# Optimization experiments

Hardware: AMD Instinct MI355X
Metric: run time of the kernel (lower is better)

## Reference

```python
import jax, jax.numpy as jnp
import numpy as np


def setup_inputs() -> dict:
    key = jax.random.key(0)
    k1, k2, k3 = jax.random.split(key, 3)
    T, H, F, E = 8192, 1024, 4096, 8
    x = jax.random.normal(k1, (T, H), dtype=jnp.float32)
    # expert weights, scaled like typical init (std ~ 1/sqrt(H))
    w1 = jax.random.normal(k2, (E, F, H), dtype=jnp.float32) * (1.0 / np.sqrt(H))
    w2 = jax.random.normal(k3, (E, F, H), dtype=jnp.float32) * (1.0 / np.sqrt(F))
    return {"x": x, "w1": w1, "w2": w2, "num_experts": E}


def reference(x, w1, w2, num_experts):
    # x: [T, H] tokens already permuted/grouped by expert (dMoE convention),
    # equal capacity per expert. w1, w2: [E, F, H].
    T, H = x.shape
    E = num_experts
    cap = T // E
    xe = x.reshape(E, cap, H)  # [E, cap, H]
    # sdd(x, w1.t(), topo): per-expert x_e @ w1_e^T -> [E, cap, F]
    h = jnp.einsum('ech,efh->ecf', xe, w1)
    # megablocks uses tanh-approximate gelu
    h = jax.nn.gelu(h, approximate=True)
    # dsd(gelu(h), w2): per-expert h_e @ w2_e -> [E, cap, H]
    out = jnp.einsum('ecf,efh->ech', h, w2)
    return out.reshape(T, H)
```

## Files before the change

kernel.cpp:

```cpp
#include <hip/hip_runtime.h>
#include <cstdint>
#include <cstddef>

typedef unsigned short u16;
typedef __attribute__((ext_vector_type(8))) short bf16x8;
typedef __attribute__((ext_vector_type(4))) float f32x4;
typedef __attribute__((ext_vector_type(8))) unsigned short u16x8;

#define T_TOK 8192
#define H_DIM 1024
#define F_DIM 4096
#define E_NUM 8
#define CAP (T_TOK / E_NUM)

__device__ __forceinline__ u16 f2bf(float f) {
  union { float f; uint32_t u; } v; v.f = f;
  uint32_t r = v.u + 0x7FFFu + ((v.u >> 16) & 1u);
  return (u16)(r >> 16);
}

__device__ __forceinline__ float gelu_tanh(float x) {
  float z2 = 1.5957691216057308f * (x + 0.044715f * x * x * x);
  float e = __expf(z2);
  return x * (1.0f - 1.0f / (e + 1.0f));
}

__device__ __forceinline__ void async_copy16(const void* gsrc, void* ldst) {
  __builtin_amdgcn_global_load_lds(
      (const __attribute__((address_space(1))) uint32_t*)gsrc,
      (__attribute__((address_space(3))) uint32_t*)ldst, 16, 0, 0);
}

__device__ __forceinline__ void wgbar() {
  asm volatile("" ::: "memory");
  __builtin_amdgcn_s_barrier();
  asm volatile("" ::: "memory");
}

template <int N> __device__ __forceinline__ void vm_wait() {
  if constexpr (N == 0) asm volatile("s_waitcnt vmcnt(0)" ::: "memory");
  else if constexpr (N == 3) asm volatile("s_waitcnt vmcnt(3)" ::: "memory");
  else if constexpr (N == 4) asm volatile("s_waitcnt vmcnt(4)" ::: "memory");
}

__global__ __launch_bounds__(256) void k_convert(const float* __restrict__ src,
                                                 u16* __restrict__ dst, long n) {
  long i = ((long)blockIdx.x * 256 + threadIdx.x) * 8;
  long stride = (long)gridDim.x * 256 * 8;
  for (; i < n; i += stride) {
    const float4 a = *(const float4*)(src + i);
    const float4 b = *(const float4*)(src + i + 4);
    u16x8 o;
    o[0] = f2bf(a.x); o[1] = f2bf(a.y); o[2] = f2bf(a.z); o[3] = f2bf(a.w);
    o[4] = f2bf(b.x); o[5] = f2bf(b.y); o[6] = f2bf(b.z); o[7] = f2bf(b.w);
    *(u16x8*)(dst + i) = o;
  }
}

__global__ __launch_bounds__(256) void k_transpose_w2(const float* __restrict__ w2,
                                                      u16* __restrict__ w2t) {
  __shared__ float tile[32][33];
  const int ntH = H_DIM / 32;
  const int ntF = F_DIM / 32;
  int bid = blockIdx.x;
  int e = bid / (ntF * ntH);
  int r = bid % (ntF * ntH);
  int f0 = (r / ntH) * 32;
  int h0 = (r % ntH) * 32;
  const float* src = w2 + (size_t)e * F_DIM * H_DIM;
  u16* dst = w2t + (size_t)e * H_DIM * F_DIM;
  int col = threadIdx.x & 31;
  int row8 = threadIdx.x >> 5;
#pragma unroll
  for (int i = 0; i < 4; i++) {
    int row = row8 + i * 8;
    tile[row][col] = src[(size_t)(f0 + row) * H_DIM + h0 + col];
  }
  __syncthreads();
#pragma unroll
  for (int i = 0; i < 4; i++) {
    int row = row8 + i * 8;
    dst[(size_t)(h0 + row) * F_DIM + f0 + col] = f2bf(tile[col][row]);
  }
}

template <int BN, int WM, int WN, int NTM, int NTN, int NT, bool GELU>
__global__ __launch_bounds__(512, 2) void k_gemm8(const u16* __restrict__ Ag,
                                                  const u16* __restrict__ Bg,
                                                  void* __restrict__ Cg) {
  constexpr int K = NT * 64;
  constexpr int FM = 256 / (WM * 16);
  constexpr int FN = BN / (WN * 16);
  constexpr int FMH = FM / 2;
  constexpr int PA = 256 * 32;
  constexpr int PB = BN * 32;
  constexpr int ABOFF = 4 * PA;
  constexpr int BSTG = (BN * 32 * 2) / (512 * 16);
  constexpr int VMC = 2 + BSTG;
  constexpr int NTOT = NTN * BN;

  __shared__ __align__(16) u16 lds[ABOFF + 4 * PB];

  const int tid = threadIdx.x;
  const int lane = tid & 63;
  const int wave = tid >> 6;
  const int wm = wave / WN;
  const int wn = wave % WN;

  constexpr int NWG = NTM * NTN;
  const int wg = ((int)blockIdx.x & 7) * (NWG / 8) + ((int)blockIdx.x >> 3);
  constexpr int NSN = NTN / 4;
  const int sup = wg >> 4, win = wg & 15;
  const int mt = (sup / NSN) * 4 + (win >> 2);
  const int nt_ = (sup % NSN) * 4 + (win & 3);

  const int e = mt >> 2;
  const u16* Ae = Ag + (size_t)mt * 256 * K;
  const u16* Be = Bg + (size_t)e * NTOT * K + (size_t)nt_ * BN * K;

  const int srow = lane >> 2;
  const int kswz = (((lane & 3) ^ ((lane >> 3) & 3)) << 3);

  auto stageA = [&](int t, int kh) {
    u16* dst0 = &lds[((t & 1) * 2 + kh) * PA];
    const u16* src = Ae + (size_t)(t * 64 + kh * 32 + kswz);
#pragma unroll
    for (int j = 0; j < 2; ++j) {
      const int cr = (2 * wave + j) * 16 + srow;
      async_copy16(src + (size_t)cr * K, dst0 + (2 * wave + j) * 512);
    }
  };
  auto stageB = [&](int t, int kh) {
    u16* dst0 = &lds[ABOFF + ((t & 1) * 2 + kh) * PB];
    const u16* src = Be + (size_t)(t * 64 + kh * 32 + kswz);
#pragma unroll
    for (int j = 0; j < BSTG; ++j) {
      const int cr = (BSTG * wave + j) * 16 + srow;
      async_copy16(src + (size_t)cr * K, dst0 + (BSTG * wave + j) * 512);
    }
  };

  const int frow = lane & 15;
  const int fslot = (((lane >> 4) ^ ((lane >> 1) & 3)) << 3);

  f32x4 acc[FM][FN] = {};

  stageA(0, 0); stageB(0, 0); stageA(0, 1); stageB(0, 1);
  stageA(1, 0); stageB(1, 0);
  vm_wait<VMC>();
  wgbar();

  for (int t = 0; t < NT; ++t) {
    const bool s01 = (t < NT - 1);
    const bool s23 = (t < NT - 2);
    bf16x8 af[FMH], bfr[FN];
#pragma unroll
    for (int q = 0; q < 4; ++q) {
      const int kh = q >> 1, mh = q & 1;
      const u16* pa = &lds[((t & 1) * 2 + kh) * PA];
      const u16* pb = &lds[ABOFF + ((t & 1) * 2 + kh) * PB];
      if (mh == 0) {
#pragma unroll
        for (int i = 0; i < FN; ++i) {
          const int r = wn * (BN / WN) + i * 16 + frow;
          bfr[i] = *(const bf16x8*)&pb[r * 32 + fslot];
        }
      }
#pragma unroll
      for (int i = 0; i < FMH; ++i) {
        const int r = wm * (256 / WM) + (mh * FMH + i) * 16 + frow;
        af[i] = *(const bf16x8*)&pa[r * 32 + fslot];
      }
      if (q == 0) { if (s01) stageA(t + 1, 1); }
      else if (q == 1) { if (s01) stageB(t + 1, 1); }
      else if (q == 2) { if (s23) stageA(t + 2, 0); }
      else { if (s23) stageB(t + 2, 0); }
      wgbar();
      asm volatile("s_waitcnt lgkmcnt(0)" ::: "memory");
      __builtin_amdgcn_sched_barrier(0);
      __builtin_amdgcn_s_setprio(1);
#pragma unroll
      for (int i = 0; i < FMH; ++i)
#pragma unroll
        for (int fn = 0; fn < FN; ++fn)
          acc[mh * FMH + i][fn] = __builtin_amdgcn_mfma_f32_16x16x32_bf16(
              af[i], bfr[fn], acc[mh * FMH + i][fn], 0, 0, 0);
      __builtin_amdgcn_s_setprio(0);
      if (q == 3) {
        if (s23) vm_wait<VMC>(); else vm_wait<0>();
      }
      wgbar();
    }
  }

  const int lr = (lane >> 4) * 4;
  const int lc = lane & 15;
  const size_t Crow0 = (size_t)mt * 256 + wm * (256 / WM);
  const int Ccol0 = nt_ * BN + wn * (BN / WN);
  if constexpr (GELU) {
    u16* Cp = (u16*)Cg;
#pragma unroll
    for (int fm = 0; fm < FM; ++fm)
#pragma unroll
      for (int fn = 0; fn < FN; ++fn) {
        const int col = Ccol0 + fn * 16 + lc;
#pragma unroll
        for (int r = 0; r < 4; ++r) {
          const size_t row = Crow0 + fm * 16 + lr + r;
          Cp[row * NTOT + col] = f2bf(gelu_tanh(acc[fm][fn][r]));
        }
      }
  } else {
    float* Cp = (float*)Cg;
#pragma unroll
    for (int fm = 0; fm < FM; ++fm)
#pragma unroll
      for (int fn = 0; fn < FN; ++fn) {
        const int col = Ccol0 + fn * 16 + lc;
#pragma unroll
        for (int r = 0; r < 4; ++r) {
          const size_t row = Crow0 + fm * 16 + lr + r;
          Cp[row * NTOT + col] = acc[fm][fn][r];
        }
      }
  }
}

extern "C" void kernel_launch(void* const* d_in, const int* in_sizes, int n_in,
                              void* d_out, int out_size, void* d_ws, size_t ws_size,
                              hipStream_t stream) {
  const float* x = (const float*)d_in[0];
  const float* w1 = (const float*)d_in[1];
  const float* w2 = (const float*)d_in[2];

  u16* ws_x = (u16*)d_ws;
  u16* ws_w1 = ws_x + (size_t)T_TOK * H_DIM;
  u16* ws_w2t = ws_w1 + (size_t)E_NUM * F_DIM * H_DIM;
  u16* ws_h = ws_w2t + (size_t)E_NUM * H_DIM * F_DIM;
  const size_t need =
      ((size_t)T_TOK * H_DIM + 2 * (size_t)E_NUM * F_DIM * H_DIM + (size_t)T_TOK * F_DIM) * 2;
  if (ws_size < need) return;

  k_convert<<<1024, 256, 0, stream>>>(x, ws_x, (long)T_TOK * H_DIM);
  k_convert<<<2048, 256, 0, stream>>>(w1, ws_w1, (long)E_NUM * F_DIM * H_DIM);
  k_transpose_w2<<<E_NUM * (F_DIM / 32) * (H_DIM / 32), 256, 0, stream>>>(w2, ws_w2t);

  k_gemm8<256, 2, 4, 32, 16, 16, true><<<512, 512, 0, stream>>>(ws_x, ws_w1, ws_h);
  k_gemm8<128, 4, 2, 32, 8, 64, false><<<256, 512, 0, stream>>>(ws_h, ws_w2t, d_out);
}
```

Baseline: 256.2 us.

## Restructure GEMM main loop pipeline with two-phase variant for second GEMM

Rewrites the k_gemm8 main loop into explicit read/MFMA helpers and adds a template flag choosing a four-phase or two-phase schedule per k-half. The down-projection GEMM now uses two phases, loading all A fragments at once and issuing A and B prefetches together, which halves the barriers per iteration. Waits on vmcnt now cover two outstanding stage pairs rather than one, so loads can run further ahead of compute. The cost is more live A-fragment registers in the two-phase path, which could pressure occupancy at two workgroups per CU.

```diff
diff --git a/kernel.cpp b/kernel.cpp
--- a/kernel.cpp
+++ b/kernel.cpp
@@ -41,6 +41,8 @@
   if constexpr (N == 0) asm volatile("s_waitcnt vmcnt(0)" ::: "memory");
   else if constexpr (N == 3) asm volatile("s_waitcnt vmcnt(3)" ::: "memory");
   else if constexpr (N == 4) asm volatile("s_waitcnt vmcnt(4)" ::: "memory");
+  else if constexpr (N == 6) asm volatile("s_waitcnt vmcnt(6)" ::: "memory");
+  else if constexpr (N == 8) asm volatile("s_waitcnt vmcnt(8)" ::: "memory");
 }
 
 __global__ __launch_bounds__(256) void k_convert(const float* __restrict__ src,
@@ -84,19 +86,19 @@
   }
 }
 
-template <int BN, int WM, int WN, int NTM, int NTN, int NT, bool GELU>
+template <int BN, int WM, int WN, int NTM, int NTN, int NT, bool GELU, bool PH4>
 __global__ __launch_bounds__(512, 2) void k_gemm8(const u16* __restrict__ Ag,
                                                   const u16* __restrict__ Bg,
                                                   void* __restrict__ Cg) {
   constexpr int K = NT * 64;
   constexpr int FM = 256 / (WM * 16);
   constexpr int FN = BN / (WN * 16);
-  constexpr int FMH = FM / 2;
+  constexpr int AFN = PH4 ? FM / 2 : FM;
   constexpr int PA = 256 * 32;
   constexpr int PB = BN * 32;
   constexpr int ABOFF = 4 * PA;
   constexpr int BSTG = (BN * 32 * 2) / (512 * 16);
-  constexpr int VMC = 2 + BSTG;
+  constexpr int PAIR = 2 + BSTG;
   constexpr int NTOT = NTN * BN;
 
   __shared__ __align__(16) u16 lds[ABOFF + 4 * PB];
@@ -144,51 +146,78 @@
   const int fslot = (((lane >> 4) ^ ((lane >> 1) & 3)) << 3);
 
   f32x4 acc[FM][FN] = {};
+  bf16x8 af[AFN], bfr[FN];
+
+  auto rdB = [&](int t, int kh) {
+    const u16* pb = &lds[ABOFF + ((t & 1) * 2 + kh) * PB];
+#pragma unroll
+    for (int i = 0; i < FN; ++i) {
+      const int r = wn * (BN / WN) + i * 16 + frow;
+      bfr[i] = *(const bf16x8*)&pb[r * 32 + fslot];
+    }
+  };
+  auto rdA = [&](int t, int kh, int mh) {
+    const u16* pa = &lds[((t & 1) * 2 + kh) * PA];
+#pragma unroll
+    for (int i = 0; i < AFN; ++i) {
+      const int r = wm * (256 / WM) + (mh * AFN + i) * 16 + frow;
+      af[i] = *(const bf16x8*)&pa[r * 32 + fslot];
+    }
+  };
+  auto domfma = [&](int mh) {
+    __builtin_amdgcn_s_setprio(1);
+#pragma unroll
+    for (int i = 0; i < AFN; ++i)
+#pragma unroll
+      for (int fn = 0; fn < FN; ++fn)
+        acc[mh * AFN + i][fn] = __builtin_amdgcn_mfma_f32_16x16x32_bf16(
+            af[i], bfr[fn], acc[mh * AFN + i][fn], 0, 0, 0);
+    __builtin_amdgcn_s_setprio(0);
+  };
 
   stageA(0, 0); stageB(0, 0); stageA(0, 1); stageB(0, 1);
   stageA(1, 0); stageB(1, 0);
-  vm_wait<VMC>();
+  vm_wait<2 * PAIR>();
   wgbar();
 
   for (int t = 0; t < NT; ++t) {
-    const bool s01 = (t < NT - 1);
-    const bool s23 = (t < NT - 2);
-    bf16x8 af[FMH], bfr[FN];
-#pragma unroll
-    for (int q = 0; q < 4; ++q) {
-      const int kh = q >> 1, mh = q & 1;
-      const u16* pa = &lds[((t & 1) * 2 + kh) * PA];
-      const u16* pb = &lds[ABOFF + ((t & 1) * 2 + kh) * PB];
-      if (mh == 0) {
-#pragma unroll
-        for (int i = 0; i < FN; ++i) {
-          const int r = wn * (BN / WN) + i * 16 + frow;
-          bfr[i] = *(const bf16x8*)&pb[r * 32 + fslot];
-        }
-      }
-#pragma unroll
-      for (int i = 0; i < FMH; ++i) {
-        const int r = wm * (256 / WM) + (mh * FMH + i) * 16 + frow;
-        af[i] = *(const bf16x8*)&pa[r * 32 + fslot];
-      }
-      if (q == 0) { if (s01) stageA(t + 1, 1); }
-      else if (q == 1) { if (s01) stageB(t + 1, 1); }
-      else if (q == 2) { if (s23) stageA(t + 2, 0); }
-      else { if (s23) stageB(t + 2, 0); }
-      wgbar();
-      asm volatile("s_waitcnt lgkmcnt(0)" ::: "memory");
-      __builtin_amdgcn_sched_barrier(0);
-      __builtin_amdgcn_s_setprio(1);
-#pragma unroll
-      for (int i = 0; i < FMH; ++i)
-#pragma unroll
-        for (int fn = 0; fn < FN; ++fn)
-          acc[mh * FMH + i][fn] = __builtin_amdgcn_mfma_f32_16x16x32_bf16(
-              af[i], bfr[fn], acc[mh * FMH + i][fn], 0, 0, 0);
-      __builtin_amdgcn_s_setprio(0);
-      if (q == 3) {
-        if (s23) vm_wait<VMC>(); else vm_wait<0>();
-      }
+    if constexpr (PH4) {
+      if (t < NT - 1) stageA(t + 1, 1);
+      rdB(t, 0); rdA(t, 0, 0);
+      wgbar(); __builtin_amdgcn_sched_barrier(0);
+      domfma(0);
+      wgbar();
+      if (t < NT - 1) stageB(t + 1, 1);
+      rdA(t, 0, 1);
+      wgbar(); __builtin_amdgcn_sched_barrier(0);
+      domfma(1);
+      if (t < NT - 1) vm_wait<2 * PAIR>(); else vm_wait<0>();
+      wgbar();
+      if (t < NT - 2) stageA(t + 2, 0);
+      rdB(t, 1); rdA(t, 1, 0);
+      wgbar(); __builtin_amdgcn_sched_barrier(0);
+      domfma(0);
+      wgbar();
+      if (t < NT - 2) stageB(t + 2, 0);
+      rdA(t, 1, 1);
+      wgbar(); __builtin_amdgcn_sched_barrier(0);
+      domfma(1);
+      if (t < NT - 2) vm_wait<2 * PAIR>();
+      else if (t == NT - 2) vm_wait<PAIR>();
+      wgbar();
+    } else {
+      if (t < NT - 1) { stageA(t + 1, 1); stageB(t + 1, 1); }
+      rdB(t, 0); rdA(t, 0, 0);
+      wgbar(); __builtin_amdgcn_sched_barrier(0);
+      domfma(0);
+      if (t < NT - 1) vm_wait<2 * PAIR>(); else vm_wait<0>();
+      wgbar();
+      if (t < NT - 2) { stageA(t + 2, 0); stageB(t + 2, 0); }
+      rdB(t, 1); rdA(t, 1, 0);
+      wgbar(); __builtin_amdgcn_sched_barrier(0);
+      domfma(0);
+      if (t < NT - 2) vm_wait<2 * PAIR>();
+      else if (t == NT - 2) vm_wait<PAIR>();
       wgbar();
     }
   }
@@ -245,6 +274,6 @@
   k_convert<<<2048, 256, 0, stream>>>(w1, ws_w1, (long)E_NUM * F_DIM * H_DIM);
   k_transpose_w2<<<E_NUM * (F_DIM / 32) * (H_DIM / 32), 256, 0, stream>>>(w2, ws_w2t);
 
-  k_gemm8<256, 2, 4, 32, 16, 16, true><<<512, 512, 0, stream>>>(ws_x, ws_w1, ws_h);
-  k_gemm8<128, 4, 2, 32, 8, 64, false><<<256, 512, 0, stream>>>(ws_h, ws_w2t, d_out);
-}
+  k_gemm8<256, 2, 4, 32, 16, 16, true, true><<<512, 512, 0, stream>>>(ws_x, ws_w1, ws_h);
+  k_gemm8<128, 4, 2, 32, 8, 64, false, false><<<256, 512, 0, stream>>>(ws_h, ws_w2t, d_out);
+}
```

Result: no change. 258.9 us (+1.1%).

## Switch GEMMs to 32x32x16 MFMA with register double-buffered LDS fragment prefetch

Applied to the files above, without the earlier changes.

Replaces the 16x16x32 MFMA tiles with 32x32x16 bf16 MFMAs so each wave uses fewer, larger matrix instructions with better operand reuse. Fragments for the next phase are read from LDS into a double-buffered register set before the current MFMAs issue, with partial lgkmcnt waits so LDS latency overlaps compute. The second GEMM changes its tile shape from 256x128 to 128x256 with a single M split. Register pressure grows (f32x16 accumulators plus double-buffered fragments) and the output write pattern changes.

```diff
diff --git a/kernel.cpp b/kernel.cpp
--- a/kernel.cpp
+++ b/kernel.cpp
@@ -4,7 +4,7 @@
 
 typedef unsigned short u16;
 typedef __attribute__((ext_vector_type(8))) short bf16x8;
-typedef __attribute__((ext_vector_type(4))) float f32x4;
+typedef __attribute__((ext_vector_type(16))) float f32x16;
 typedef __attribute__((ext_vector_type(8))) unsigned short u16x8;
 
 #define T_TOK 8192
@@ -13,6 +13,8 @@
 #define E_NUM 8
 #define CAP (T_TOK / E_NUM)
 
+template <int I> struct IC { static constexpr int v = I; };
+
 __device__ __forceinline__ u16 f2bf(float f) {
   union { float f; uint32_t u; } v; v.f = f;
   uint32_t r = v.u + 0x7FFFu + ((v.u >> 16) & 1u);
@@ -40,7 +42,18 @@
 template <int N> __device__ __forceinline__ void vm_wait() {
   if constexpr (N == 0) asm volatile("s_waitcnt vmcnt(0)" ::: "memory");
   else if constexpr (N == 3) asm volatile("s_waitcnt vmcnt(3)" ::: "memory");
-  else if constexpr (N == 4) asm volatile("s_waitcnt vmcnt(4)" ::: "memory");
+  else if constexpr (N == 6) asm volatile("s_waitcnt vmcnt(6)" ::: "memory");
+  else if constexpr (N == 8) asm volatile("s_waitcnt vmcnt(8)" ::: "memory");
+}
+
+template <int N> __device__ __forceinline__ void lgkm_wait() {
+  if constexpr (N == 0) asm volatile("s_waitcnt lgkmcnt(0)" ::: "memory");
+  else if constexpr (N == 4) asm volatile("s_waitcnt lgkmcnt(4)" ::: "memory");
+  else if constexpr (N == 8) asm volatile("s_waitcnt lgkmcnt(8)" ::: "memory");
+}
+
+__device__ __forceinline__ f32x16 mfma32(bf16x8 a, bf16x8 b, f32x16 c) {
+  return __builtin_amdgcn_mfma_f32_32x32x16_bf16(a, b, c, 0, 0, 0);
 }
 
 __global__ __launch_bounds__(256) void k_convert(const float* __restrict__ src,
@@ -84,28 +97,35 @@
   }
 }
 
-template <int BN, int WM, int WN, int NTM, int NTN, int NT, bool GELU>
-__global__ __launch_bounds__(512, 2) void k_gemm8(const u16* __restrict__ Ag,
-                                                  const u16* __restrict__ Bg,
-                                                  void* __restrict__ Cg) {
+template <int BM, int BN, int MSPLIT, int NTN, int NT, bool GELU>
+__global__ __launch_bounds__(512, 2) void k_gemm(const u16* __restrict__ Ag,
+                                                 const u16* __restrict__ Bg,
+                                                 void* __restrict__ Cg) {
   constexpr int K = NT * 64;
-  constexpr int FM = 256 / (WM * 16);
-  constexpr int FN = BN / (WN * 16);
-  constexpr int FMH = FM / 2;
-  constexpr int PA = 256 * 32;
+  constexpr int WROWS = BM / 2;
+  constexpr int WCOLS = 64;
+  constexpr int MF = WROWS / 32;
+  constexpr int MFH = MF / MSPLIT;
+  constexpr int NF = 2;
+  constexpr int NPH = 2 * MSPLIT;
+  constexpr int PA = BM * 32;
   constexpr int PB = BN * 32;
   constexpr int ABOFF = 4 * PA;
-  constexpr int BSTG = (BN * 32 * 2) / (512 * 16);
-  constexpr int VMC = 2 + BSTG;
+  constexpr int JA = BM / 128;
+  constexpr int JB = BN / 128;
   constexpr int NTOT = NTN * BN;
+  constexpr int NTM = T_TOK / BM;
+  constexpr int MT_PER_E = CAP / BM;
+  constexpr int VMS = 3 * MSPLIT;
+  constexpr int VMP = (MSPLIT == 2) ? 8 : 3;
 
   __shared__ __align__(16) u16 lds[ABOFF + 4 * PB];
 
   const int tid = threadIdx.x;
   const int lane = tid & 63;
   const int wave = tid >> 6;
-  const int wm = wave / WN;
-  const int wn = wave % WN;
+  const int wm = wave >> 2;
+  const int wn = wave & 3;
 
   constexpr int NWG = NTM * NTN;
   const int wg = ((int)blockIdx.x & 7) * (NWG / 8) + ((int)blockIdx.x >> 3);
@@ -114,8 +134,8 @@
   const int mt = (sup / NSN) * 4 + (win >> 2);
   const int nt_ = (sup % NSN) * 4 + (win & 3);
 
-  const int e = mt >> 2;
-  const u16* Ae = Ag + (size_t)mt * 256 * K;
+  const int e = mt / MT_PER_E;
+  const u16* Ae = Ag + (size_t)mt * BM * K;
   const u16* Be = Bg + (size_t)e * NTOT * K + (size_t)nt_ * BN * K;
 
   const int srow = lane >> 2;
@@ -125,105 +145,132 @@
     u16* dst0 = &lds[((t & 1) * 2 + kh) * PA];
     const u16* src = Ae + (size_t)(t * 64 + kh * 32 + kswz);
 #pragma unroll
-    for (int j = 0; j < 2; ++j) {
-      const int cr = (2 * wave + j) * 16 + srow;
-      async_copy16(src + (size_t)cr * K, dst0 + (2 * wave + j) * 512);
+    for (int j = 0; j < JA; ++j) {
+      const int cr = (JA * wave + j) * 16 + srow;
+      async_copy16(src + (size_t)cr * K, dst0 + (JA * wave + j) * 512);
     }
   };
   auto stageB = [&](int t, int kh) {
     u16* dst0 = &lds[ABOFF + ((t & 1) * 2 + kh) * PB];
     const u16* src = Be + (size_t)(t * 64 + kh * 32 + kswz);
 #pragma unroll
-    for (int j = 0; j < BSTG; ++j) {
-      const int cr = (BSTG * wave + j) * 16 + srow;
-      async_copy16(src + (size_t)cr * K, dst0 + (BSTG * wave + j) * 512);
-    }
-  };
-
-  const int frow = lane & 15;
-  const int fslot = (((lane >> 4) ^ ((lane >> 1) & 3)) << 3);
-
-  f32x4 acc[FM][FN] = {};
+    for (int j = 0; j < JB; ++j) {
+      const int cr = (JB * wave + j) * 16 + srow;
+      async_copy16(src + (size_t)cr * K, dst0 + (JB * wave + j) * 512);
+    }
+  };
+
+  const int lane31 = lane & 31;
+  const int khi = lane >> 5;
+  const int swz = (lane >> 1) & 3;
+
+  f32x16 acc[MF][NF] = {};
+  bf16x8 afb[2][MFH][2];
+  bf16x8 bfb[2][NF][2];
+
+  auto rdA = [&](auto BUF, auto MH, int tpar, int kh) {
+    const u16* pa = &lds[(tpar * 2 + kh) * PA];
+#pragma unroll
+    for (int i = 0; i < MFH; ++i)
+#pragma unroll
+      for (int ks = 0; ks < 2; ++ks)
+        afb[BUF.v][i][ks] = *(const bf16x8*)&pa[
+            (wm * WROWS + (MH.v * MFH + i) * 32 + lane31) * 32 +
+            (((khi + 2 * ks) ^ swz) << 3)];
+  };
+  auto rdB = [&](auto KHB, int tpar, int kh) {
+    const u16* pb = &lds[ABOFF + (tpar * 2 + kh) * PB];
+#pragma unroll
+    for (int j = 0; j < NF; ++j)
+#pragma unroll
+      for (int ks = 0; ks < 2; ++ks)
+        bfb[KHB.v][j][ks] = *(const bf16x8*)&pb[
+            (wn * WCOLS + j * 32 + lane31) * 32 +
+            (((khi + 2 * ks) ^ swz) << 3)];
+  };
 
   stageA(0, 0); stageB(0, 0); stageA(0, 1); stageB(0, 1);
   stageA(1, 0); stageB(1, 0);
-  vm_wait<VMC>();
+  vm_wait<VMP>();
   wgbar();
+  rdA(IC<0>{}, IC<0>{}, 0, 0);
+  rdB(IC<0>{}, 0, 0);
+
+  auto phaseF = [&](auto QC, int t, bool hasNext, bool has2, bool tailVM) {
+    constexpr int Q = QC.v;
+    constexpr int KH = (MSPLIT == 2) ? (Q >> 1) : Q;
+    constexpr int MH = (MSPLIT == 2) ? (Q & 1) : 0;
+    constexpr int QN = (Q + 1) % NPH;
+    constexpr int KHN = (MSPLIT == 2) ? (QN >> 1) : QN;
+    constexpr int MHN = (MSPLIT == 2) ? (QN & 1) : 0;
+    constexpr bool RB = (MHN == 0);
+    constexpr int ABW = (Q + 1) & 1, ABR = Q & 1;
+    constexpr bool WRAP = (Q == NPH - 1);
+    constexpr int NJUST = MFH * 2 + (RB ? NF * 2 : 0);
+    const int tN = WRAP ? t + 1 : t;
+    const bool doRead = !WRAP || hasNext;
+    if (doRead) {
+      rdA(IC<ABW>{}, IC<MHN>{}, tN & 1, KHN);
+      if constexpr (RB) rdB(IC<KHN>{}, tN & 1, KHN);
+      lgkm_wait<NJUST>();
+    } else {
+      lgkm_wait<0>();
+    }
+    if constexpr (MSPLIT == 2) {
+      if constexpr (Q == 0) { if (hasNext) stageA(t + 1, 1); }
+      else if constexpr (Q == 1) { if (hasNext) stageB(t + 1, 1); }
+      else if constexpr (Q == 2) { if (has2) stageA(t + 2, 0); }
+      else { if (has2) stageB(t + 2, 0); }
+    } else {
+      if constexpr (Q == 0) { if (hasNext) { stageA(t + 1, 1); stageB(t + 1, 1); } }
+      else { if (has2) { stageA(t + 2, 0); stageB(t + 2, 0); } }
+    }
+    __builtin_amdgcn_sched_barrier(0);
+    __builtin_amdgcn_s_setprio(1);
+#pragma unroll
+    for (int i = 0; i < MFH; ++i)
+#pragma unroll
+      for (int j = 0; j < NF; ++j)
+#pragma unroll
+        for (int ks = 0; ks < 2; ++ks)
+          acc[MH * MFH + i][j] = mfma32(afb[ABR][i][ks], bfb[KH][j][ks],
+                                        acc[MH * MFH + i][j]);
+    __builtin_amdgcn_s_setprio(0);
+    if constexpr (MSPLIT == 1 || (Q & 1) == 0) {
+      if (tailVM) vm_wait<0>(); else vm_wait<VMS>();
+    }
+    wgbar();
+  };
 
   for (int t = 0; t < NT; ++t) {
-    const bool s01 = (t < NT - 1);
-    const bool s23 = (t < NT - 2);
-    bf16x8 af[FMH], bfr[FN];
-#pragma unroll
-    for (int q = 0; q < 4; ++q) {
-      const int kh = q >> 1, mh = q & 1;
-      const u16* pa = &lds[((t & 1) * 2 + kh) * PA];
-      const u16* pb = &lds[ABOFF + ((t & 1) * 2 + kh) * PB];
-      if (mh == 0) {
-#pragma unroll
-        for (int i = 0; i < FN; ++i) {
-          const int r = wn * (BN / WN) + i * 16 + frow;
-          bfr[i] = *(const bf16x8*)&pb[r * 32 + fslot];
+    const bool hasNext = (t < NT - 1);
+    const bool has2 = (t < NT - 2);
+    const bool tailVM = (t >= NT - 3);
+    phaseF(IC<0>{}, t, hasNext, has2, tailVM);
+    phaseF(IC<1>{}, t, hasNext, has2, tailVM);
+    if constexpr (MSPLIT == 2) {
+      phaseF(IC<2>{}, t, hasNext, has2, tailVM);
+      phaseF(IC<3>{}, t, hasNext, has2, tailVM);
+    }
+  }
+
+  const size_t Crow0 = (size_t)mt * BM + wm * WROWS;
+  const int Ccol0 = nt_ * BN + wn * WCOLS;
+#pragma unroll
+  for (int fm = 0; fm < MF; ++fm)
+#pragma unroll
+    for (int fn = 0; fn < NF; ++fn) {
+      const int col = Ccol0 + fn * 32 + lane31;
+#pragma unroll
+      for (int r = 0; r < 16; ++r) {
+        const size_t row = Crow0 + fm * 32 + (r & 3) + 8 * (r >> 2) + 4 * khi;
+        if constexpr (GELU) {
+          ((u16*)Cg)[row * NTOT + col] = f2bf(gelu_tanh(acc[fm][fn][r]));
+        } else {
+          ((float*)Cg)[row * NTOT + col] = acc[fm][fn][r];
         }
       }
-#pragma unroll
-      for (int i = 0; i < FMH; ++i) {
-        const int r = wm * (256 / WM) + (mh * FMH + i) * 16 + frow;
-        af[i] = *(const bf16x8*)&pa[r * 32 + fslot];
-      }
-      if (q == 0) { if (s01) stageA(t + 1, 1); }
-      else if (q == 1) { if (s01) stageB(t + 1, 1); }
-      else if (q == 2) { if (s23) stageA(t + 2, 0); }
-      else { if (s23) stageB(t + 2, 0); }
-      wgbar();
-      asm volatile("s_waitcnt lgkmcnt(0)" ::: "memory");
-      __builtin_amdgcn_sched_barrier(0);
-      __builtin_amdgcn_s_setprio(1);
-#pragma unroll
-      for (int i = 0; i < FMH; ++i)
-#pragma unroll
-        for (int fn = 0; fn < FN; ++fn)
-          acc[mh * FMH + i][fn] = __builtin_amdgcn_mfma_f32_16x16x32_bf16(
-              af[i], bfr[fn], acc[mh * FMH + i][fn], 0, 0, 0);
-      __builtin_amdgcn_s_setprio(0);
-      if (q == 3) {
-        if (s23) vm_wait<VMC>(); else vm_wait<0>();
-      }
-      wgbar();
-    }
-  }
-
-  const int lr = (lane >> 4) * 4;
-  const int lc = lane & 15;
-  const size_t Crow0 = (size_t)mt * 256 + wm * (256 / WM);
-  const int Ccol0 = nt_ * BN + wn * (BN / WN);
-  if constexpr (GELU) {
-    u16* Cp = (u16*)Cg;
-#pragma unroll
-    for (int fm = 0; fm < FM; ++fm)
-#pragma unroll
-      for (int fn = 0; fn < FN; ++fn) {
-        const int col = Ccol0 + fn * 16 + lc;
-#pragma unroll
-        for (int r = 0; r < 4; ++r) {
-          const size_t row = Crow0 + fm * 16 + lr + r;
-          Cp[row * NTOT + col] = f2bf(gelu_tanh(acc[fm][fn][r]));
-        }
-      }
-  } else {
-    float* Cp = (float*)Cg;
-#pragma unroll
-    for (int fm = 0; fm < FM; ++fm)
-#pragma unroll
-      for (int fn = 0; fn < FN; ++fn) {
-        const int col = Ccol0 + fn * 16 + lc;
-#pragma unroll
-        for (int r = 0; r < 4; ++r) {
-          const size_t row = Crow0 + fm * 16 + lr + r;
-          Cp[row * NTOT + col] = acc[fm][fn][r];
-        }
-      }
-  }
+    }
 }
 
 extern "C" void kernel_launch(void* const* d_in, const int* in_sizes, int n_in,
@@ -245,6 +292,6 @@
   k_convert<<<2048, 256, 0, stream>>>(w1, ws_w1, (long)E_NUM * F_DIM * H_DIM);
   k_transpose_w2<<<E_NUM * (F_DIM / 32) * (H_DIM / 32), 256, 0, stream>>>(w2, ws_w2t);
 
-  k_gemm8<256, 2, 4, 32, 16, 16, true><<<512, 512, 0, stream>>>(ws_x, ws_w1, ws_h);
-  k_gemm8<128, 4, 2, 32, 8, 64, false><<<256, 512, 0, stream>>>(ws_h, ws_w2t, d_out);
-}
+  k_gemm<256, 256, 2, 16, 16, true><<<512, 512, 0, stream>>>(ws_x, ws_w1, ws_h);
+  k_gemm<128, 256, 1, 4, 64, false><<<256, 512, 0, stream>>>(ws_h, ws_w2t, d_out);
+}
```

After: 276.7 us. 1.08x slower.
